# Kernel optimization log

Measured on AMD Instinct MI355X. Metric: run time of the kernel, lower is better.

The kernel has to match this reference:

```python
import jax, jax.numpy as jnp
import numpy as np


def setup_inputs() -> dict:
    key = jax.random.key(0)
    k1, k2 = jax.random.split(key)
    data = jax.random.normal(k1, (32, 1, 224, 224), dtype=jnp.float32)
    weight = jax.random.normal(k2, (64, 1, 3, 3), dtype=jnp.float32)
    return {"data": data, "weight": weight}


def reference(data, weight):
    # Valid (no padding), stride-1, dilation-1, groups-1 cross-correlation,
    # identical math to the loop-unrolled broadcast-multiply-sum in the source.
    # data: [B, 1, H, W], weight: [O, 1, kH, kW] -> out: [B, O, H-kH+1, W-kW+1]
    return jax.lax.conv_general_dilated(
        data,
        weight,
        window_strides=(1, 1),
        padding="VALID",
        dimension_numbers=("NCHW", "OIHW", "NCHW"),
    )
```

## Files before the change

### kernel.cpp

```cpp
#include <hip/hip_runtime.h>
#include <hip/hip_bf16.h>


#define IN_H 224
#define IN_W 224
#define OUT_H 222
#define OUT_W 222
#define OUT_C 64
#define BATCH 32
#define XPAIRS (OUT_W / 2)

__global__ __launch_bounds__(256) void conv3x3_kernel(
    const float* __restrict__ in, const float* __restrict__ wt,
    float* __restrict__ out) {
  const int tid = blockIdx.x * blockDim.x + threadIdx.x;
  const int total = BATCH * OUT_H * XPAIRS;
  if (tid >= total) return;

  const int xp = tid % XPAIRS;
  const int t  = tid / XPAIRS;
  const int y  = t % OUT_H;
  const int b  = t / OUT_H;
  const int x  = xp * 2;

  const float* ip = in + ((size_t)b * IN_H + y) * IN_W + x;
  float2 r0a = *(const float2*)(ip);
  float2 r0b = *(const float2*)(ip + 2);
  float2 r1a = *(const float2*)(ip + IN_W);
  float2 r1b = *(const float2*)(ip + IN_W + 2);
  float2 r2a = *(const float2*)(ip + 2 * IN_W);
  float2 r2b = *(const float2*)(ip + 2 * IN_W + 2);

  const float i00 = r0a.x, i01 = r0a.y, i02 = r0b.x, i03 = r0b.y;
  const float i10 = r1a.x, i11 = r1a.y, i12 = r1b.x, i13 = r1b.y;
  const float i20 = r2a.x, i21 = r2a.y, i22 = r2b.x, i23 = r2b.y;

  float* op = out + ((size_t)b * OUT_C) * (OUT_H * OUT_W)
                  + (size_t)y * OUT_W + x;

  #pragma unroll 4
  for (int ch = 0; ch < OUT_C; ++ch) {
    const float* w = wt + ch * 9;
    const float w0 = w[0], w1 = w[1], w2 = w[2];
    const float w3 = w[3], w4 = w[4], w5 = w[5];
    const float w6 = w[6], w7 = w[7], w8 = w[8];

    float o0 = i00 * w0;
    float o1 = i01 * w0;
    o0 = fmaf(i01, w1, o0);  o1 = fmaf(i02, w1, o1);
    o0 = fmaf(i02, w2, o0);  o1 = fmaf(i03, w2, o1);
    o0 = fmaf(i10, w3, o0);  o1 = fmaf(i11, w3, o1);
    o0 = fmaf(i11, w4, o0);  o1 = fmaf(i12, w4, o1);
    o0 = fmaf(i12, w5, o0);  o1 = fmaf(i13, w5, o1);
    o0 = fmaf(i20, w6, o0);  o1 = fmaf(i21, w6, o1);
    o0 = fmaf(i21, w7, o0);  o1 = fmaf(i22, w7, o1);
    o0 = fmaf(i22, w8, o0);  o1 = fmaf(i23, w8, o1);

    *(float2*)op = make_float2(o0, o1);
    op += OUT_H * OUT_W;
  }
}

extern "C" void kernel_launch(void* const* d_in, const int* in_sizes, int n_in,
                              void* d_out, int out_size, void* d_ws, size_t ws_size,
                              hipStream_t stream) {
  const float* data   = (const float*)d_in[0];
  const float* weight = (const float*)d_in[1];
  float* out = (float*)d_out;

  const int total = BATCH * OUT_H * XPAIRS;
  const int block = 256;
  const int grid  = (total + block - 1) / block;
  conv3x3_kernel<<<grid, block, 0, stream>>>(data, weight, out);
}
```

Measured before the change: 439.0 us.

## Split output channels across grid and compute four outputs per thread

Each thread now computes 4 horizontal outputs for only 2 output channels, and the grid's y and z dimensions index channel pairs and batch. Before, each thread looped over all 64 channels. Inputs are loaded as float4 plus a float2 halo, and the last column group stores only 2 outputs. This gives far more parallelism and spreads the output writes across many concurrent threads, at the cost of re-reading the input 32 times, which mostly hits in cache.

```diff
diff --git a/kernel.cpp b/kernel.cpp
--- a/kernel.cpp
+++ b/kernel.cpp
@@ -8,56 +8,61 @@
 #define OUT_W 222
 #define OUT_C 64
 #define BATCH 32
-#define XPAIRS (OUT_W / 2)
+#define XG 56
+#define PLANE (OUT_H * OUT_W)
+#define THREADS_PER_PLANE (OUT_H * XG)
 
 __global__ __launch_bounds__(256) void conv3x3_kernel(
     const float* __restrict__ in, const float* __restrict__ wt,
     float* __restrict__ out) {
-  const int tid = blockIdx.x * blockDim.x + threadIdx.x;
-  const int total = BATCH * OUT_H * XPAIRS;
-  if (tid >= total) return;
-
-  const int xp = tid % XPAIRS;
-  const int t  = tid / XPAIRS;
-  const int y  = t % OUT_H;
-  const int b  = t / OUT_H;
-  const int x  = xp * 2;
+  const int t = blockIdx.x * blockDim.x + threadIdx.x;
+  if (t >= THREADS_PER_PLANE) return;
+  const int xg = t % XG;
+  const int y  = t / XG;
+  const int x  = xg * 4;
+  const int b  = blockIdx.z;
+  const int ch0 = blockIdx.y * 2;
 
   const float* ip = in + ((size_t)b * IN_H + y) * IN_W + x;
-  float2 r0a = *(const float2*)(ip);
-  float2 r0b = *(const float2*)(ip + 2);
-  float2 r1a = *(const float2*)(ip + IN_W);
-  float2 r1b = *(const float2*)(ip + IN_W + 2);
-  float2 r2a = *(const float2*)(ip + 2 * IN_W);
-  float2 r2b = *(const float2*)(ip + 2 * IN_W + 2);
+  const float4 a0 = *(const float4*)(ip);
+  const float4 a1 = *(const float4*)(ip + IN_W);
+  const float4 a2 = *(const float4*)(ip + 2 * IN_W);
 
-  const float i00 = r0a.x, i01 = r0a.y, i02 = r0b.x, i03 = r0b.y;
-  const float i10 = r1a.x, i11 = r1a.y, i12 = r1b.x, i13 = r1b.y;
-  const float i20 = r2a.x, i21 = r2a.y, i22 = r2b.x, i23 = r2b.y;
+  const bool full = (xg != XG - 1);
+  float e00 = 0.f, e01 = 0.f, e10 = 0.f, e11 = 0.f, e20 = 0.f, e21 = 0.f;
+  if (full) {
+    const float2 e0 = *(const float2*)(ip + 4);
+    const float2 e1 = *(const float2*)(ip + IN_W + 4);
+    const float2 e2 = *(const float2*)(ip + 2 * IN_W + 4);
+    e00 = e0.x; e01 = e0.y; e10 = e1.x; e11 = e1.y; e20 = e2.x; e21 = e2.y;
+  }
 
-  float* op = out + ((size_t)b * OUT_C) * (OUT_H * OUT_W)
-                  + (size_t)y * OUT_W + x;
+  const float rin[3][6] = {
+    {a0.x, a0.y, a0.z, a0.w, e00, e01},
+    {a1.x, a1.y, a1.z, a1.w, e10, e11},
+    {a2.x, a2.y, a2.z, a2.w, e20, e21},
+  };
 
-  #pragma unroll 4
-  for (int ch = 0; ch < OUT_C; ++ch) {
-    const float* w = wt + ch * 9;
-    const float w0 = w[0], w1 = w[1], w2 = w[2];
-    const float w3 = w[3], w4 = w[4], w5 = w[5];
-    const float w6 = w[6], w7 = w[7], w8 = w[8];
+  float* op = out + (size_t)(b * OUT_C + ch0) * PLANE + (size_t)y * OUT_W + x;
 
-    float o0 = i00 * w0;
-    float o1 = i01 * w0;
-    o0 = fmaf(i01, w1, o0);  o1 = fmaf(i02, w1, o1);
-    o0 = fmaf(i02, w2, o0);  o1 = fmaf(i03, w2, o1);
-    o0 = fmaf(i10, w3, o0);  o1 = fmaf(i11, w3, o1);
-    o0 = fmaf(i11, w4, o0);  o1 = fmaf(i12, w4, o1);
-    o0 = fmaf(i12, w5, o0);  o1 = fmaf(i13, w5, o1);
-    o0 = fmaf(i20, w6, o0);  o1 = fmaf(i21, w6, o1);
-    o0 = fmaf(i21, w7, o0);  o1 = fmaf(i22, w7, o1);
-    o0 = fmaf(i22, w8, o0);  o1 = fmaf(i23, w8, o1);
-
-    *(float2*)op = make_float2(o0, o1);
-    op += OUT_H * OUT_W;
+  #pragma unroll
+  for (int c = 0; c < 2; ++c) {
+    const float* w = wt + (ch0 + c) * 9;
+    float o[4] = {0.f, 0.f, 0.f, 0.f};
+    #pragma unroll
+    for (int r = 0; r < 3; ++r) {
+      #pragma unroll
+      for (int k = 0; k < 3; ++k) {
+        const float wv = w[r * 3 + k];
+        #pragma unroll
+        for (int j = 0; j < 4; ++j)
+          o[j] = fmaf(rin[r][j + k], wv, o[j]);
+      }
+    }
+    *(float2*)(op)     = make_float2(o[0], o[1]);
+    if (full)
+      *(float2*)(op + 2) = make_float2(o[2], o[3]);
+    op += PLANE;
   }
 }
 
@@ -68,8 +73,6 @@
   const float* weight = (const float*)d_in[1];
   float* out = (float*)d_out;
 
-  const int total = BATCH * OUT_H * XPAIRS;
-  const int block = 256;
-  const int grid  = (total + block - 1) / block;
-  conv3x3_kernel<<<grid, block, 0, stream>>>(data, weight, out);
+  dim3 grid((THREADS_PER_PLANE + 255) / 256, OUT_C / 2, BATCH);
+  conv3x3_kernel<<<grid, 256, 0, stream>>>(data, weight, out);
 }
```

New measurement: 436.6 us. Within noise of the previous version (-0.5%).
